# Performance work log

Measured on AMD Instinct MI355X. Metric: run time of the kernel, lower is better.

The kernel has to match this reference:

```python
import jax, jax.numpy as jnp
import numpy as np
from jax.ops import segment_sum, segment_max

N, E, C, L = 50000, 600000, 128, 4
H = 2 * C  # GENConv MLP hidden = expansion(2) * in_channels
EPS_MSG = 1e-7   # GENConv message eps
EPS_LN = 1e-5    # PyG LayerNorm eps (graph mode)
EPS_GN = 1e-5    # GraphNorm eps
EPS_SM = 1e-16   # PyG softmax denominator eps


def setup_inputs() -> dict:
    key = jax.random.key(0)
    ks = jax.random.split(key, 8)
    s = 0.05
    return dict(
        x=jax.random.normal(ks[0], (N, C), jnp.float32),
        src=jax.random.randint(ks[1], (E,), 0, N),
        dst=jax.random.randint(ks[2], (E,), 0, N),
        W1=jax.random.normal(ks[3], (L, C, H), jnp.float32) * s,
        b1=jnp.zeros((L, H), jnp.float32),
        ln_w=jnp.ones((L, H), jnp.float32),
        ln_b=jnp.zeros((L, H), jnp.float32),
        W2=jax.random.normal(ks[4], (L, H, C), jnp.float32) * s,
        b2=jnp.zeros((L, C), jnp.float32),
        t=jnp.ones((L,), jnp.float32),      # learn_t=True, init t=1.0
        gn_w=jnp.ones((L, C), jnp.float32),
        gn_b=jnp.zeros((L, C), jnp.float32),
        gn_a=jnp.ones((L, C), jnp.float32),  # GraphNorm mean_scale
        lin_w=jax.random.normal(ks[5], (C, 1), jnp.float32) * s,
        lin_b=jnp.zeros((1,), jnp.float32),
    )


def graph_norm(x, w, b, a):
    # single graph: per-channel mean over nodes
    mean = x.mean(axis=0)
    out = x - a * mean
    var = (out * out).mean(axis=0)
    return w * out / jnp.sqrt(var + EPS_GN) + b


def gen_conv(x, src, dst, t, W1, b1, ln_w, ln_b, W2, b2):
    # message: relu(x_j) + eps  (no edge_attr)
    msg = jax.nn.relu(x[src]) + EPS_MSG           # [E, C]
    z = t * msg
    m = segment_max(z, dst, num_segments=N)        # [N, C]
    ex = jnp.exp(z - m[dst])
    den = segment_sum(ex, dst, num_segments=N) + EPS_SM
    alpha = ex / den[dst]                          # per-node per-channel softmax
    agg = segment_sum(msg * alpha, dst, num_segments=N)  # [N, C]
    out = agg + x                                  # root add
    # MLP([C, 2C, C]) with PyG LayerNorm (graph mode) + ReLU between layers
    h = out @ W1 + b1                              # [N, H]
    h = (h - h.mean()) / (h.std() + EPS_LN)        # graph-mode LN: scalar stats
    h = jax.nn.relu(h * ln_w + ln_b)
    return h @ W2 + b2                             # [N, C]


def reference(x, src, dst, W1, b1, ln_w, ln_b, W2, b2, t, gn_w, gn_b, gn_a, lin_w, lin_b):
    for l in range(L):
        # DeepGCNLayer block='res+': norm -> act -> (dropout=0) -> conv, residual add
        h = graph_norm(x, gn_w[l], gn_b[l], gn_a[l])
        h = jax.nn.relu(h)
        h = gen_conv(h, src, dst, t[l], W1[l], b1[l], ln_w[l], ln_b[l], W2[l], b2[l])
        x = x + h
    return x @ lin_w + lin_b                       # [N, 1]
```

## Files before the change

kernel.cpp:

```cpp
#include <hip/hip_runtime.h>

#define C_DIM 128
#define H_DIM 256
#define L_NUM 4

typedef __attribute__((ext_vector_type(8))) short bf16x8;
typedef __attribute__((ext_vector_type(4))) float f32x4;

__device__ __forceinline__ unsigned short f2bf(float f){
  unsigned u = __builtin_bit_cast(unsigned, f);
  u = u + 0x7FFFu + ((u >> 16) & 1u);
  return (unsigned short)(u >> 16);
}
__device__ __forceinline__ float bf2f(unsigned short b){
  return __builtin_bit_cast(float, ((unsigned)b) << 16);
}
__device__ __forceinline__ float fexp2(float x){
#if __has_builtin(__builtin_amdgcn_exp2f)
  return __builtin_amdgcn_exp2f(x);
#else
  float r; asm("v_exp_f32 %0, %1" : "=v"(r) : "v"(x)); return r;
#endif
}

__global__ void k_hist(const int* __restrict__ dst, int* __restrict__ cnt, int E){
  for (int e = blockIdx.x*blockDim.x + threadIdx.x; e < E; e += gridDim.x*blockDim.x)
    atomicAdd(cnt + dst[e], 1);
}

__global__ void k_scan_local(const int* __restrict__ cnt, int* __restrict__ rp,
                             int* __restrict__ bsum, int N){
  __shared__ int tmp[256];
  int t = threadIdx.x; int i = blockIdx.x*256 + t;
  int v = (i < N) ? cnt[i] : 0;
  tmp[t] = v; __syncthreads();
  for (int off = 1; off < 256; off <<= 1){
    int x = (t >= off) ? tmp[t-off] : 0; __syncthreads();
    tmp[t] += x; __syncthreads();
  }
  if (i < N) rp[i] = tmp[t] - v;
  if (t == 255) bsum[blockIdx.x] = tmp[t];
}

__global__ void k_scan_bsums(const int* __restrict__ bsum, int* __restrict__ boff, int nb){
  __shared__ int tmp[256];
  int t = threadIdx.x;
  int v = (t < nb) ? bsum[t] : 0;
  tmp[t] = v; __syncthreads();
  for (int off = 1; off < 256; off <<= 1){
    int x = (t >= off) ? tmp[t-off] : 0; __syncthreads();
    tmp[t] += x; __syncthreads();
  }
  if (t < nb) boff[t] = tmp[t] - v;
}

__global__ void k_scan_add(int* __restrict__ rp, const int* __restrict__ boff, int N, int E){
  int i = blockIdx.x*256 + threadIdx.x;
  if (i < N) rp[i] += boff[blockIdx.x];
  if (i == 0) rp[N] = E;
}

__global__ void k_scatter(const int* __restrict__ src, const int* __restrict__ dst,
                          const int* __restrict__ rp, int* __restrict__ cnt,
                          int* __restrict__ csrc, int E){
  for (int e = blockIdx.x*blockDim.x + threadIdx.x; e < E; e += gridDim.x*blockDim.x){
    int d = dst[e];
    int pos = rp[d] + atomicAdd(cnt + d, 1);
    csrc[pos] = src[e];
  }
}

__global__ void k_wconv(const float* __restrict__ W1, const float* __restrict__ W2,
                        unsigned short* __restrict__ W1t, unsigned short* __restrict__ W2t){
  int i = blockIdx.x*blockDim.x + threadIdx.x;
  if (i >= L_NUM*C_DIM*H_DIM) return;
  int l = i >> 15, r = i & 32767;
  { int k = r >> 8, n = r & 255;  W1t[l*32768 + n*128 + k] = f2bf(W1[i]); }
  { int k = r >> 7, n = r & 127;  W2t[l*32768 + n*256 + k] = f2bf(W2[i]); }
}

__global__ void k_stat0(const float* __restrict__ X, float* __restrict__ part, int NB, int N){
  int t = threadIdx.x; int c = t & 127; int half = t >> 7;
  int r0 = blockIdx.x*128, rend = min(r0 + 128, N);
  float s = 0.f, s2 = 0.f;
  for (int r = r0 + half; r < rend; r += 2){
    float v = X[r*C_DIM + c]; s += v; s2 += v*v;
  }
  __shared__ float a1[256], a2[256];
  a1[t] = s; a2[t] = s2; __syncthreads();
  if (t < 128){
    part[t*NB + blockIdx.x]       = a1[t] + a1[t+128];
    part[(128+t)*NB + blockIdx.x] = a2[t] + a2[t+128];
  }
}

__global__ void k_gn_coef(const float* __restrict__ part, int NB, int nb,
                          const float* __restrict__ gw, const float* __restrict__ gb,
                          const float* __restrict__ ga, const float* __restrict__ tptr, int l,
                          float* __restrict__ coef, int N){
  int c = blockIdx.x;
  int t = threadIdx.x;
  float s = 0.f, s2 = 0.f;
  for (int i = t; i < nb; i += 256){
    s  += part[c*NB + i];
    s2 += part[(128+c)*NB + i];
  }
  __shared__ float sh1[256], sh2[256];
  sh1[t] = s; sh2[t] = s2; __syncthreads();
  for (int off = 128; off; off >>= 1){
    if (t < off){ sh1[t] += sh1[t+off]; sh2[t] += sh2[t+off]; }
    __syncthreads();
  }
  if (t == 0){
    float kk = tptr[l] * 1.4426950408889634f;
    float inv = 1.f/(float)N;
    float mean = sh1[0]*inv;
    float am = ga[c]*mean;
    float var = sh2[0]*inv - 2.f*am*mean + am*am;
    float scale = gw[c] * rsqrtf(var + 1e-5f);
    coef[c] = scale * kk;
    coef[128+c] = (gb[c] - scale*am) * kk;
  }
}

__global__ void k_gpre(const float* __restrict__ X, const float* __restrict__ coef,
                       unsigned* __restrict__ G2, int total4){
  int i = blockIdx.x*blockDim.x + threadIdx.x;
  if (i >= total4) return;
  int c4 = i & 31;
  float4 x = ((const float4*)X)[i];
  float4 A = ((const float4*)coef)[c4];
  float4 B = ((const float4*)coef)[32 + c4];
  float o0 = fmaxf(A.x*x.x + B.x, 0.f);
  float o1 = fmaxf(A.y*x.y + B.y, 0.f);
  float o2 = fmaxf(A.z*x.z + B.z, 0.f);
  float o3 = fmaxf(A.w*x.w + B.w, 0.f);
  uint2 pk = make_uint2((unsigned)f2bf(o0) | ((unsigned)f2bf(o1) << 16),
                        (unsigned)f2bf(o2) | ((unsigned)f2bf(o3) << 16));
  ((uint2*)G2)[i] = pk;
}

__global__ void k_agg(const unsigned* __restrict__ G, const int* __restrict__ rp,
                      const int* __restrict__ csrc, const float* __restrict__ tptr, int l,
                      unsigned short* __restrict__ U, int N){
  int wave = threadIdx.x >> 6, lane = threadIdx.x & 63;
  int n = blockIdx.x*4 + wave;
  if (n >= N) return;
  float invkk = 1.f / (tptr[l] * 1.4426950408889634f);
  int jb = rp[n], je = rp[n+1];
  float d0 = 0.f, d1 = 0.f, s0 = 0.f, s1 = 0.f;
  unsigned uo = G[(size_t)n*64 + lane];

  #define EDGE(uu) { \
    float p0 = __builtin_bit_cast(float, (uu) << 16); \
    float p1 = __builtin_bit_cast(float, (uu) & 0xffff0000u); \
    float e0 = fexp2(p0); \
    float e1 = fexp2(p1); \
    d0 += e0; d1 += e1; \
    s0 = fmaf(p0, e0, s0); s1 = fmaf(p1, e1, s1); }

  for (int base = jb; base < je; base += 64){
    int cnt = min(64, je - base);
    int myidx = (base + lane < je) ? csrc[base + lane] : 0;
    int jj = 0;
    for (; jj + 3 < cnt; jj += 4){
      int i0 = __shfl(myidx, jj);
      int i1 = __shfl(myidx, jj+1);
      int i2 = __shfl(myidx, jj+2);
      int i3 = __shfl(myidx, jj+3);
      unsigned v0 = G[(size_t)i0*64 + lane];
      unsigned v1 = G[(size_t)i1*64 + lane];
      unsigned v2 = G[(size_t)i2*64 + lane];
      unsigned v3 = G[(size_t)i3*64 + lane];
      EDGE(v0); EDGE(v1); EDGE(v2); EDGE(v3);
    }
    for (; jj < cnt; ++jj){
      unsigned u = G[(size_t)__shfl(myidx, jj)*64 + lane];
      EDGE(u);
    }
  }
  #undef EDGE

  float o0 = __builtin_bit_cast(float, uo << 16);
  float o1 = __builtin_bit_cast(float, uo & 0xffff0000u);
  float u0 = invkk * (s0/(d0 + 1e-16f) + o0) + 1e-7f;
  float u1 = invkk * (s1/(d1 + 1e-16f) + o1) + 1e-7f;
  unsigned pk = (unsigned)f2bf(u0) | ((unsigned)f2bf(u1) << 16);
  *(unsigned*)(U + n*C_DIM + lane*2) = pk;
}

__global__ void k_gemm1(const unsigned short* __restrict__ A, const unsigned short* __restrict__ Bt,
                        const float* __restrict__ b1, unsigned short* __restrict__ H1,
                        float* __restrict__ part, int M){
  __shared__ __align__(16) char smem[64*256];
  __shared__ float rbuf[8];
  const int tid = threadIdx.x;
  const int m0 = blockIdx.x * 64;
  const int wave = tid >> 6, lane = tid & 63;
  const int lr = lane & 15, lc = lane >> 4;

  bf16x8 bf[4][4];
  #pragma unroll
  for (int nf = 0; nf < 4; ++nf){
    int n = wave*64 + nf*16 + lr;
    #pragma unroll
    for (int ks = 0; ks < 4; ++ks)
      bf[nf][ks] = *(const bf16x8*)(Bt + n*128 + ks*32 + lc*8);
  }
  #pragma unroll
  for (int p = 0; p < 4; ++p){
    int idx = p*256 + tid;
    int row = idx >> 4, ch = idx & 15;
    int r = m0 + row;
    uint4 v = make_uint4(0u,0u,0u,0u);
    if (r < M) v = *(const uint4*)(A + r*128 + ch*8);
    int o = (row*256 + ch*16) ^ ((row & 7) << 4);
    *(uint4*)(smem + o) = v;
  }
  __syncthreads();

  f32x4 acc[4][4] = {};
  #pragma unroll
  for (int ks = 0; ks < 4; ++ks){
    bf16x8 a[4];
    #pragma unroll
    for (int mf = 0; mf < 4; ++mf){
      int row = mf*16 + lr;
      int o = (row*256 + ks*64 + lc*16) ^ ((row & 7) << 4);
      a[mf] = *(const bf16x8*)(smem + o);
    }
    #pragma unroll
    for (int mf = 0; mf < 4; ++mf)
      #pragma unroll
      for (int nf = 0; nf < 4; ++nf)
        acc[mf][nf] = __builtin_amdgcn_mfma_f32_16x16x32_bf16(a[mf], bf[nf][ks], acc[mf][nf], 0, 0, 0);
  }

  float s1 = 0.f, s2 = 0.f;
  #pragma unroll
  for (int mf = 0; mf < 4; ++mf){
    #pragma unroll
    for (int j = 0; j < 4; ++j){
      int r = m0 + mf*16 + lc*4 + j;
      if (r < M){
        #pragma unroll
        for (int nf = 0; nf < 4; ++nf){
          int col = wave*64 + nf*16 + lr;
          float v = acc[mf][nf][j] + b1[col];
          H1[r*H_DIM + col] = f2bf(v);
          s1 += v; s2 += v*v;
        }
      }
    }
  }
  #pragma unroll
  for (int o = 32; o; o >>= 1){ s1 += __shfl_down(s1, o); s2 += __shfl_down(s2, o); }
  if (lane == 0){ rbuf[wave] = s1; rbuf[4 + wave] = s2; }
  __syncthreads();
  if (tid == 0)
    part[blockIdx.x*2]     = rbuf[0]+rbuf[1]+rbuf[2]+rbuf[3];
  if (tid == 1)
    part[blockIdx.x*2 + 1] = rbuf[4]+rbuf[5]+rbuf[6]+rbuf[7];
}

__global__ void k_gemm2(const unsigned short* __restrict__ H1,
                        const float* __restrict__ lnpart, int nparts,
                        const float* __restrict__ lnw, const float* __restrict__ lnb,
                        const unsigned short* __restrict__ Bt, const float* __restrict__ b2,
                        const float* __restrict__ Xin, float* __restrict__ Xout,
                        float* __restrict__ part, int NB,
                        const float* __restrict__ lw, const float* __restrict__ lb,
                        float* __restrict__ out, int M){
  __shared__ __align__(16) char smem[64*512];
  __shared__ float red1[256], red2[256];
  __shared__ float colw[256], colb[256];
  __shared__ float rowdot[64];
  const int tid = threadIdx.x;
  const int m0 = blockIdx.x * 64;
  const int wave = tid >> 6, lane = tid & 63;
  const int lr = lane & 15, lc = lane >> 4;
  const bool last = (lw != nullptr);

  {
    float s1 = 0.f, s2 = 0.f;
    for (int i = tid; i < nparts; i += 256){ s1 += lnpart[2*i]; s2 += lnpart[2*i+1]; }
    red1[tid] = s1; red2[tid] = s2; __syncthreads();
    for (int o = 128; o; o >>= 1){
      if (tid < o){ red1[tid] += red1[tid+o]; red2[tid] += red2[tid+o]; }
      __syncthreads();
    }
    double NH = (double)M * (double)H_DIM;
    double mean = (double)red1[0] / NH;
    double var = (double)red2[0] / NH - mean*mean;
    double sd = sqrt(var > 0.0 ? var : 0.0);
    float denom = (float)sd + 1e-5f;
    float wv = lnw[tid] / denom;
    colw[tid] = wv;
    colb[tid] = lnb[tid] - (float)mean * wv;
    if (tid < 64) rowdot[tid] = 0.f;
    __syncthreads();
  }

  bf16x8 bf[2][8];
  #pragma unroll
  for (int nf = 0; nf < 2; ++nf){
    int n = wave*32 + nf*16 + lr;
    #pragma unroll
    for (int ks = 0; ks < 8; ++ks)
      bf[nf][ks] = *(const bf16x8*)(Bt + n*256 + ks*32 + lc*8);
  }
  #pragma unroll
  for (int p = 0; p < 8; ++p){
    int idx = (p*256 + tid)*8;
    int row = idx >> 8, col = idx & 255;
    int r = m0 + row;
    uint4 v = make_uint4(0u,0u,0u,0u);
    if (r < M) v = *(const uint4*)(H1 + r*H_DIM + col);
    unsigned short hb[8] = {(unsigned short)(v.x&0xffff),(unsigned short)(v.x>>16),
                            (unsigned short)(v.y&0xffff),(unsigned short)(v.y>>16),
                            (unsigned short)(v.z&0xffff),(unsigned short)(v.z>>16),
                            (unsigned short)(v.w&0xffff),(unsigned short)(v.w>>16)};
    unsigned outp[4];
    #pragma unroll
    for (int q = 0; q < 4; ++q){
      float f0 = fmaxf(colw[col+2*q]  *bf2f(hb[2*q])   + colb[col+2*q],   0.f);
      float f1 = fmaxf(colw[col+2*q+1]*bf2f(hb[2*q+1]) + colb[col+2*q+1], 0.f);
      outp[q] = (unsigned)f2bf(f0) | ((unsigned)f2bf(f1) << 16);
    }
    int o = (row*512 + col*2) ^ ((row & 7) << 4);
    *(uint4*)(smem + o) = make_uint4(outp[0],outp[1],outp[2],outp[3]);
  }
  __syncthreads();

  f32x4 acc[4][2] = {};
  #pragma unroll
  for (int ks = 0; ks < 8; ++ks){
    bf16x8 a[4];
    #pragma unroll
    for (int mf = 0; mf < 4; ++mf){
      int row = mf*16 + lr;
      int o = (row*512 + ks*64 + lc*16) ^ ((row & 7) << 4);
      a[mf] = *(const bf16x8*)(smem + o);
    }
    #pragma unroll
    for (int mf = 0; mf < 4; ++mf)
      #pragma unroll
      for (int nf = 0; nf < 2; ++nf)
        acc[mf][nf] = __builtin_amdgcn_mfma_f32_16x16x32_bf16(a[mf], bf[nf][ks], acc[mf][nf], 0, 0, 0);
  }

  float sA[2] = {0.f, 0.f}, sB[2] = {0.f, 0.f};
  #pragma unroll
  for (int mf = 0; mf < 4; ++mf){
    #pragma unroll
    for (int j = 0; j < 4; ++j){
      int r = m0 + mf*16 + lc*4 + j;
      if (r < M){
        float p = 0.f;
        #pragma unroll
        for (int nf = 0; nf < 2; ++nf){
          int col = wave*32 + nf*16 + lr;
          float v = Xin[r*C_DIM + col] + acc[mf][nf][j] + b2[col];
          if (!last){
            Xout[r*C_DIM + col] = v;
            sA[nf] += v; sB[nf] += v*v;
          } else {
            p += v * lw[col];
          }
        }
        if (last){
          p += __shfl_xor(p, 1); p += __shfl_xor(p, 2);
          p += __shfl_xor(p, 4); p += __shfl_xor(p, 8);
          if (lr == 0) atomicAdd(&rowdot[r - m0], p);
        }
      }
    }
  }
  if (!last){
    #pragma unroll
    for (int nf = 0; nf < 2; ++nf){
      sA[nf] += __shfl_xor(sA[nf], 16); sA[nf] += __shfl_xor(sA[nf], 32);
      sB[nf] += __shfl_xor(sB[nf], 16); sB[nf] += __shfl_xor(sB[nf], 32);
    }
    if (lane < 16){
      #pragma unroll
      for (int nf = 0; nf < 2; ++nf){
        int col = wave*32 + nf*16 + lr;
        part[col*NB + blockIdx.x]       = sA[nf];
        part[(128+col)*NB + blockIdx.x] = sB[nf];
      }
    }
  } else {
    __syncthreads();
    if (tid < 64 && m0 + tid < M) out[m0 + tid] = rowdot[tid] + lb[0];
  }
}

extern "C" void kernel_launch(void* const* d_in, const int* in_sizes, int n_in,
                              void* d_out, int out_size, void* d_ws, size_t ws_size,
                              hipStream_t stream){
  const float* x    = (const float*)d_in[0];
  const int*   src  = (const int*)d_in[1];
  const int*   dst  = (const int*)d_in[2];
  const float* W1   = (const float*)d_in[3];
  const float* b1   = (const float*)d_in[4];
  const float* lnw  = (const float*)d_in[5];
  const float* lnb  = (const float*)d_in[6];
  const float* W2   = (const float*)d_in[7];
  const float* b2   = (const float*)d_in[8];
  const float* tpt  = (const float*)d_in[9];
  const float* gnw  = (const float*)d_in[10];
  const float* gnb  = (const float*)d_in[11];
  const float* gna  = (const float*)d_in[12];
  const float* linw = (const float*)d_in[13];
  const float* linb = (const float*)d_in[14];
  (void)n_in; (void)out_size; (void)ws_size;
  const int N = in_sizes[0] / C_DIM;
  const int E = in_sizes[1];
  float* out = (float*)d_out;

  const int gmw = (N + 63)/64;
  const int S0  = (N + 127)/128;
  const int NB  = gmw;

  char* wsp = (char*)d_ws; size_t off = 0;
  auto alloc = [&](size_t b)->char*{ char* p = wsp + off; off += (b + 255) & ~(size_t)255; return p; };
  int* cnt          = (int*)alloc((size_t)N*4);
  int* rp           = (int*)alloc((size_t)(N+1)*4);
  int* bsum         = (int*)alloc(1024);
  int* boff         = (int*)alloc(1024);
  float* gncoef     = (float*)alloc(1024);
  float* lnpart     = (float*)alloc((size_t)gmw*2*4);
  float* part       = (float*)alloc((size_t)NB*256*4);
  int* csrc         = (int*)alloc((size_t)E*4);
  unsigned short* W1t = (unsigned short*)alloc((size_t)L_NUM*C_DIM*H_DIM*2);
  unsigned short* W2t = (unsigned short*)alloc((size_t)L_NUM*C_DIM*H_DIM*2);
  unsigned* g       = (unsigned*)alloc((size_t)N*C_DIM*2);
  unsigned short* U = (unsigned short*)alloc((size_t)N*C_DIM*2);
  unsigned short* h1 = (unsigned short*)alloc((size_t)N*H_DIM*2);
  float* xc         = (float*)alloc((size_t)N*C_DIM*4);

  const int SB = (N + 255)/256;
  hipMemsetAsync(cnt, 0, (size_t)N*4, stream);
  k_hist<<<1024, 256, 0, stream>>>(dst, cnt, E);
  k_scan_local<<<SB, 256, 0, stream>>>(cnt, rp, bsum, N);
  k_scan_bsums<<<1, 256, 0, stream>>>(bsum, boff, SB);
  k_scan_add<<<SB, 256, 0, stream>>>(rp, boff, N, E);
  hipMemsetAsync(cnt, 0, (size_t)N*4, stream);
  k_scatter<<<1024, 256, 0, stream>>>(src, dst, rp, cnt, csrc, E);
  k_wconv<<<(L_NUM*C_DIM*H_DIM + 255)/256, 256, 0, stream>>>(W1, W2, W1t, W2t);
  k_stat0<<<S0, 256, 0, stream>>>(x, part, NB, N);

  for (int l = 0; l < L_NUM; ++l){
    int nb = (l == 0) ? S0 : gmw;
    const float* Xin = (l == 0) ? x : xc;
    bool lastL = (l == L_NUM - 1);
    k_gn_coef<<<128, 256, 0, stream>>>(part, NB, nb, gnw + l*C_DIM, gnb + l*C_DIM, gna + l*C_DIM, tpt, l, gncoef, N);
    k_gpre<<<(N*32 + 255)/256, 256, 0, stream>>>(Xin, gncoef, g, N*32);
    k_agg<<<(N + 3)/4, 256, 0, stream>>>(g, rp, csrc, tpt, l, U, N);
    k_gemm1<<<gmw, 256, 0, stream>>>(U, W1t + (size_t)l*C_DIM*H_DIM, b1 + l*H_DIM, h1, lnpart, N);
    k_gemm2<<<gmw, 256, 0, stream>>>(h1, lnpart, gmw, lnw + l*H_DIM, lnb + l*H_DIM,
                                     W2t + (size_t)l*C_DIM*H_DIM, b2 + l*C_DIM,
                                     Xin, xc, part, NB,
                                     lastL ? linw : nullptr, linb, out, N);
  }
}
```

Before: 441.1 us.

## Merge setup kernels into one launch and shrink aggregation blocks

Weight conversion, the initial column statistics and the edge histogram now run as block ranges of a single kernel instead of three separate launches. The second memset of the count array is folded into the scan-add kernel. The aggregation kernel now uses two waves per 128-thread block instead of four per 256-thread block. These changes aim to cut launch count and serial gaps in setup, and to improve scheduling granularity in aggregation. The trade-off is more small blocks.

```diff
diff --git a/kernel.cpp b/kernel.cpp
--- a/kernel.cpp
+++ b/kernel.cpp
@@ -23,9 +23,37 @@
 #endif
 }
 
-__global__ void k_hist(const int* __restrict__ dst, int* __restrict__ cnt, int E){
-  for (int e = blockIdx.x*blockDim.x + threadIdx.x; e < E; e += gridDim.x*blockDim.x)
-    atomicAdd(cnt + dst[e], 1);
+__global__ void k_pre(const float* __restrict__ W1, const float* __restrict__ W2,
+                      unsigned short* __restrict__ W1t, unsigned short* __restrict__ W2t,
+                      const float* __restrict__ X, float* __restrict__ part, int NB,
+                      const int* __restrict__ dst, int* __restrict__ cnt,
+                      int N, int E, int S0){
+  __shared__ float a1[256], a2[256];
+  int b = blockIdx.x;
+  if (b < 512){
+    int i = b*256 + threadIdx.x;
+    int l = i >> 15, r = i & 32767;
+    { int k = r >> 8, n = r & 255;  W1t[l*32768 + n*128 + k] = f2bf(W1[i]); }
+    { int k = r >> 7, n = r & 127;  W2t[l*32768 + n*256 + k] = f2bf(W2[i]); }
+  } else if (b < 512 + S0){
+    int chunk = b - 512;
+    int t = threadIdx.x; int c = t & 127; int half = t >> 7;
+    int r0 = chunk*128, rend = min(r0 + 128, N);
+    float s = 0.f, s2 = 0.f;
+    for (int r = r0 + half; r < rend; r += 2){
+      float v = X[r*C_DIM + c]; s += v; s2 += v*v;
+    }
+    a1[t] = s; a2[t] = s2; __syncthreads();
+    if (t < 128){
+      part[t*NB + chunk]       = a1[t] + a1[t+128];
+      part[(128+t)*NB + chunk] = a2[t] + a2[t+128];
+    }
+  } else {
+    int nb = gridDim.x - 512 - S0;
+    int bb = b - 512 - S0;
+    for (int e = bb*256 + threadIdx.x; e < E; e += nb*256)
+      atomicAdd(cnt + dst[e], 1);
+  }
 }
 
 __global__ void k_scan_local(const int* __restrict__ cnt, int* __restrict__ rp,
@@ -54,9 +82,10 @@
   if (t < nb) boff[t] = tmp[t] - v;
 }
 
-__global__ void k_scan_add(int* __restrict__ rp, const int* __restrict__ boff, int N, int E){
+__global__ void k_scan_add(int* __restrict__ rp, const int* __restrict__ boff,
+                           int* __restrict__ cnt, int N, int E){
   int i = blockIdx.x*256 + threadIdx.x;
-  if (i < N) rp[i] += boff[blockIdx.x];
+  if (i < N){ rp[i] += boff[blockIdx.x]; cnt[i] = 0; }
   if (i == 0) rp[N] = E;
 }
 
@@ -67,30 +96,6 @@
     int d = dst[e];
     int pos = rp[d] + atomicAdd(cnt + d, 1);
     csrc[pos] = src[e];
-  }
-}
-
-__global__ void k_wconv(const float* __restrict__ W1, const float* __restrict__ W2,
-                        unsigned short* __restrict__ W1t, unsigned short* __restrict__ W2t){
-  int i = blockIdx.x*blockDim.x + threadIdx.x;
-  if (i >= L_NUM*C_DIM*H_DIM) return;
-  int l = i >> 15, r = i & 32767;
-  { int k = r >> 8, n = r & 255;  W1t[l*32768 + n*128 + k] = f2bf(W1[i]); }
-  { int k = r >> 7, n = r & 127;  W2t[l*32768 + n*256 + k] = f2bf(W2[i]); }
-}
-
-__global__ void k_stat0(const float* __restrict__ X, float* __restrict__ part, int NB, int N){
-  int t = threadIdx.x; int c = t & 127; int half = t >> 7;
-  int r0 = blockIdx.x*128, rend = min(r0 + 128, N);
-  float s = 0.f, s2 = 0.f;
-  for (int r = r0 + half; r < rend; r += 2){
-    float v = X[r*C_DIM + c]; s += v; s2 += v*v;
-  }
-  __shared__ float a1[256], a2[256];
-  a1[t] = s; a2[t] = s2; __syncthreads();
-  if (t < 128){
-    part[t*NB + blockIdx.x]       = a1[t] + a1[t+128];
-    part[(128+t)*NB + blockIdx.x] = a2[t] + a2[t+128];
   }
 }
 
@@ -144,7 +149,7 @@
                       const int* __restrict__ csrc, const float* __restrict__ tptr, int l,
                       unsigned short* __restrict__ U, int N){
   int wave = threadIdx.x >> 6, lane = threadIdx.x & 63;
-  int n = blockIdx.x*4 + wave;
+  int n = blockIdx.x*2 + wave;
   if (n >= N) return;
   float invkk = 1.f / (tptr[l] * 1.4426950408889634f);
   int jb = rp[n], je = rp[n+1];
@@ -442,14 +447,11 @@
 
   const int SB = (N + 255)/256;
   hipMemsetAsync(cnt, 0, (size_t)N*4, stream);
-  k_hist<<<1024, 256, 0, stream>>>(dst, cnt, E);
+  k_pre<<<512 + S0 + 1024, 256, 0, stream>>>(W1, W2, W1t, W2t, x, part, NB, dst, cnt, N, E, S0);
   k_scan_local<<<SB, 256, 0, stream>>>(cnt, rp, bsum, N);
   k_scan_bsums<<<1, 256, 0, stream>>>(bsum, boff, SB);
-  k_scan_add<<<SB, 256, 0, stream>>>(rp, boff, N, E);
-  hipMemsetAsync(cnt, 0, (size_t)N*4, stream);
+  k_scan_add<<<SB, 256, 0, stream>>>(rp, boff, cnt, N, E);
   k_scatter<<<1024, 256, 0, stream>>>(src, dst, rp, cnt, csrc, E);
-  k_wconv<<<(L_NUM*C_DIM*H_DIM + 255)/256, 256, 0, stream>>>(W1, W2, W1t, W2t);
-  k_stat0<<<S0, 256, 0, stream>>>(x, part, NB, N);
 
   for (int l = 0; l < L_NUM; ++l){
     int nb = (l == 0) ? S0 : gmw;
@@ -457,7 +459,7 @@
     bool lastL = (l == L_NUM - 1);
     k_gn_coef<<<128, 256, 0, stream>>>(part, NB, nb, gnw + l*C_DIM, gnb + l*C_DIM, gna + l*C_DIM, tpt, l, gncoef, N);
     k_gpre<<<(N*32 + 255)/256, 256, 0, stream>>>(Xin, gncoef, g, N*32);
-    k_agg<<<(N + 3)/4, 256, 0, stream>>>(g, rp, csrc, tpt, l, U, N);
+    k_agg<<<(N + 1)/2, 128, 0, stream>>>(g, rp, csrc, tpt, l, U, N);
     k_gemm1<<<gmw, 256, 0, stream>>>(U, W1t + (size_t)l*C_DIM*H_DIM, b1 + l*H_DIM, h1, lnpart, N);
     k_gemm2<<<gmw, 256, 0, stream>>>(h1, lnpart, gmw, lnw + l*H_DIM, lnb + l*H_DIM,
                                      W2t + (size_t)l*C_DIM*H_DIM, b2 + l*C_DIM,
```

Result: faster. 430.9 us (-2.3%).
